# Performance work log

Measured on AMD Instinct MI355X. Metric: run time of the kernel, lower is better.

Reference implementation:

```python
import jax, jax.numpy as jnp
import numpy as np

N, D, K = 16384, 256, 4096   # tokens, feature dim, codebook_size
GAMMA = 0.99


def setup_inputs() -> dict:
    key = jax.random.key(0)
    k1, k2, k3 = jax.random.split(key, 3)
    features = jax.random.normal(k1, (N, D), dtype=jnp.float32)
    mask = jax.random.uniform(k2, (N,)) < 0.9
    codebook = jax.random.normal(k3, (K, D), dtype=jnp.float32)  # hk RandomNormal init
    count = jnp.zeros((K,), jnp.float32)
    avg = jnp.zeros((K,), jnp.float32)
    return {"features": features, "mask": mask, "codebook": codebook,
            "count": count, "avg": avg}


def reference(features, mask, codebook, count, avg):
    sg = jax.lax.stop_gradient
    prev_codebook = codebook

    # pairwise squared distances [N, K] via ||f||^2 - 2 f.C^T + ||c||^2
    f2 = jnp.sum(features * features, axis=-1)            # [N]
    c2 = jnp.sum(codebook * codebook, axis=-1)            # [K]
    distance = f2[:, None] - 2.0 * (features @ codebook.T) + c2[None, :]
    distance = jnp.where(mask[:, None], distance, jnp.inf)

    assign_fwd = jnp.argmin(distance, axis=1)             # [N] nearest code per token
    assign_rev = jnp.argmin(distance, axis=0)             # [K] nearest token per code
    features_fwd = codebook[assign_fwd]                   # [N, D]
    features_rev = features[assign_rev]                   # [K, D]

    # straight-through estimator
    out_features = sg(features_fwd) + features - sg(features)

    total = jnp.maximum(mask.sum(), 1).astype(features.dtype)
    commitment = jnp.mean((sg(features_fwd) - features) ** 2, axis=-1)
    commitment_loss = jnp.where(mask, commitment, 0.0).sum() / total

    # scatter-add assignment counts (masked) and feature sums (unmasked, as in source)
    assignment_count = jnp.zeros((K,), jnp.float32).at[assign_fwd].add(
        mask.astype(jnp.float32))
    assignment_mask = assignment_count < 1

    count = (1.0 - GAMMA) * assignment_count + GAMMA * count
    avg = (1.0 - GAMMA) * assignment_count / total + GAMMA * avg
    alpha = jnp.exp(-avg * K * 10.0 / (1.0 - GAMMA) - 0.001)

    feat_sum = jnp.zeros_like(codebook).at[assign_fwd].add(features)  # [K, D]
    assigned_update = (GAMMA * codebook + (1.0 - GAMMA) * feat_sum)
    assigned_update = assigned_update / jnp.maximum(count[:, None], 1.0)
    unassigned_update = (1.0 - alpha)[:, None] * codebook + alpha[:, None] * features_rev
    new_codebook = jnp.where(assignment_mask[:, None], assigned_update, unassigned_update)

    # pmean(delta) is identity on a single device; final = prev + (prev - new), as in source
    codebook_delta = prev_codebook - new_codebook
    new_codebook = prev_codebook + codebook_delta

    unassigned_percent = (assignment_count > 0).mean()
    return (out_features, assign_fwd, commitment_loss, unassigned_percent,
            count, avg, new_codebook)
```

## Files before the change

### kernel.cpp

```cpp
#include <hip/hip_runtime.h>
#include <math.h>

typedef unsigned long long u64;
typedef unsigned int u32;

#define N_TOK 16384
#define DIM   256
#define KCB   4096

#define WS_ROWMIN   0
#define WS_COLMIN   131072
#define WS_CNT      163840
#define WS_CPART    180224
#define WS_TOTAL    181248
#define WS_FLAG     181252
#define WS_F2       181312
#define WS_C2       246848
#define WS_END      263232

#define OUT_FEAT    0
#define OUT_ASSIGN  4194304
#define OUT_CLOSS   4210688
#define OUT_UPCT    4210689
#define OUT_COUNT   4210690
#define OUT_AVG     4214786
#define OUT_CB      4218882

#define C_1MG 0.009999999776482582f

__device__ __forceinline__ u32 fkey(float d) {
    u32 u = __float_as_uint(d);
    return (u & 0x80000000u) ? ~u : (u | 0x80000000u);
}
__device__ __forceinline__ u64 u64min(u64 a, u64 b) { return a < b ? a : b; }
__device__ __forceinline__ u64 shflxor64(u64 v, int m) {
    int lo = __shfl_xor((int)(u32)(v & 0xFFFFFFFFULL), m, 64);
    int hi = __shfl_xor((int)(u32)(v >> 32), m, 64);
    return ((u64)(u32)hi << 32) | (u32)lo;
}
__device__ __forceinline__ bool read_mask(const void* mp, int flag, int n) {
    if (flag == 2) return ((const float*)mp)[n] != 0.0f;
    if (flag == 1) return ((const int*)mp)[n] != 0;
    return ((const unsigned char*)mp)[n] != 0;
}

__global__ void k_detect(const void* __restrict__ mp, int* __restrict__ flag) {
    if (threadIdx.x == 0) {
        const u32* w = (const u32*)mp;
        bool allf = true, alli = true, any1 = false;
        for (int i = 0; i < 64; ++i) {
            u32 x = w[i];
            if (x != 0u && x != 0x3F800000u) allf = false;
            if (x == 0x3F800000u) any1 = true;
            if (x > 1u) alli = false;
        }
        *flag = (allf && any1) ? 2 : (alli ? 1 : 0);
    }
}

__global__ __launch_bounds__(256)
void k_norms(const float* __restrict__ F, const float* __restrict__ CB,
             const void* __restrict__ mp, const int* __restrict__ flagp,
             float* __restrict__ f2, float* __restrict__ c2) {
    __shared__ float red[4];
    const int b = blockIdx.x, d = threadIdx.x;
    const float* src = (b < N_TOK) ? (F + (size_t)b * DIM) : (CB + (size_t)(b - N_TOK) * DIM);
    float v = src[d];
    float s = v * v;
#pragma unroll
    for (int m = 32; m > 0; m >>= 1) s += __shfl_xor(s, m, 64);
    if ((d & 63) == 0) red[d >> 6] = s;
    __syncthreads();
    if (d == 0) {
        float tot = red[0] + red[1] + red[2] + red[3];
        if (b < N_TOK) {
            bool msk = read_mask(mp, *flagp, b);
            f2[b] = msk ? tot : __builtin_huge_valf();
        } else {
            c2[b - N_TOK] = tot;
        }
    }
}

__global__ __launch_bounds__(256, 4)
void k_gemm(const float* __restrict__ F, const float* __restrict__ CB,
            const float* __restrict__ f2, const float* __restrict__ c2,
            u64* __restrict__ rowmin, u64* __restrict__ colmin) {
    __shared__ float As[128][32];
    __shared__ float Bs[128][32];
    __shared__ u64 colred[4][128];

    const int t = threadIdx.x;
    const int ty = t >> 4, tx = t & 15;
    const int wave = t >> 6;
    const int rowbase = blockIdx.x * 128;
    const int kbase = blockIdx.y * 128;

    float acc[8][8];
#pragma unroll
    for (int i = 0; i < 8; ++i)
#pragma unroll
        for (int j = 0; j < 8; ++j) acc[i][j] = 0.0f;

    for (int dc = 0; dc < 8; ++dc) {
        const int db = dc * 32;
#pragma unroll
        for (int i = 0; i < 4; ++i) {
            int g = t + i * 256;
            int r = g >> 3;
            int c4 = (g & 7) << 2;
            int sw = c4 ^ (((r >> 3) & 7) << 2);
            *(float4*)&As[r][sw] = *(const float4*)(F + (size_t)(rowbase + r) * DIM + db + c4);
            *(float4*)&Bs[r][sw] = *(const float4*)(CB + (size_t)(kbase + r) * DIM + db + c4);
        }
        __syncthreads();
#pragma unroll
        for (int dd = 0; dd < 32; dd += 2) {
            float2 a[8], b[8];
#pragma unroll
            for (int i = 0; i < 8; ++i)
                a[i] = *(const float2*)&As[ty * 8 + i][dd ^ ((ty & 7) << 2)];
#pragma unroll
            for (int j = 0; j < 8; ++j)
                b[j] = *(const float2*)&Bs[tx * 8 + j][dd ^ ((tx & 7) << 2)];
#pragma unroll
            for (int i = 0; i < 8; ++i)
#pragma unroll
                for (int j = 0; j < 8; ++j) {
                    acc[i][j] = fmaf(a[i].x, b[j].x, acc[i][j]);
                    acc[i][j] = fmaf(a[i].y, b[j].y, acc[i][j]);
                }
        }
        __syncthreads();
    }

    float c2k[8];
#pragma unroll
    for (int j = 0; j < 8; ++j) c2k[j] = c2[kbase + tx * 8 + j];
    u64 cbst[8];
#pragma unroll
    for (int j = 0; j < 8; ++j) cbst[j] = ~0ULL;

#pragma unroll
    for (int i = 0; i < 8; ++i) {
        const int row = rowbase + ty * 8 + i;
        const float f2r = f2[row];
        u64 rbst = ~0ULL;
#pragma unroll
        for (int j = 0; j < 8; ++j) {
            float dist = (f2r - 2.0f * acc[i][j]) + c2k[j];
            u64 hk = (u64)fkey(dist) << 32;
            rbst    = u64min(rbst, hk | (u32)(kbase + tx * 8 + j));
            cbst[j] = u64min(cbst[j], hk | (u32)row);
        }
        rbst = u64min(rbst, shflxor64(rbst, 1));
        rbst = u64min(rbst, shflxor64(rbst, 2));
        rbst = u64min(rbst, shflxor64(rbst, 4));
        rbst = u64min(rbst, shflxor64(rbst, 8));
        if (tx == 0) atomicMin(&rowmin[row], rbst);
    }

#pragma unroll
    for (int j = 0; j < 8; ++j) {
        cbst[j] = u64min(cbst[j], shflxor64(cbst[j], 16));
        cbst[j] = u64min(cbst[j], shflxor64(cbst[j], 32));
    }
    if ((t & 63) < 16) {
#pragma unroll
        for (int j = 0; j < 8; ++j) colred[wave][tx * 8 + j] = cbst[j];
    }
    __syncthreads();
    if (t < 128) {
        u64 m = u64min(u64min(colred[0][t], colred[1][t]),
                       u64min(colred[2][t], colred[3][t]));
        atomicMin(&colmin[kbase + t], m);
    }
}

__global__ __launch_bounds__(256)
void k_token(const float* __restrict__ F, const float* __restrict__ CB,
             const u64* __restrict__ rowmin, const void* __restrict__ mp,
             const int* __restrict__ flagp,
             float* __restrict__ out_feat, float* __restrict__ out_assign,
             float* __restrict__ cnt, float* __restrict__ fsum,
             float* __restrict__ cpart) {
    __shared__ float red[4];
    const int n = blockIdx.x, d = threadIdx.x;
    const int k = (int)(u32)(rowmin[n] & 0xFFFFFFFFULL);
    const float f = F[(size_t)n * DIM + d];
    const float cv = CB[(size_t)k * DIM + d];
    out_feat[(size_t)n * DIM + d] = (cv + f) - f;
    const float df = cv - f;
    float s = df * df;
#pragma unroll
    for (int m = 32; m > 0; m >>= 1) s += __shfl_xor(s, m, 64);
    if ((d & 63) == 0) red[d >> 6] = s;
    __syncthreads();
    atomicAdd(&fsum[(size_t)k * DIM + d], f);
    if (d == 0) {
        out_assign[n] = (float)k;
        bool msk = read_mask(mp, *flagp, n);
        if (msk) {
            float tot = red[0] + red[1] + red[2] + red[3];
            atomicAdd(&cnt[k], 1.0f);
            atomicAdd(&cpart[n & 255], tot * (1.0f / 256.0f));
        }
    }
}

__global__ __launch_bounds__(256)
void k_scalars(const float* __restrict__ cnt, const float* __restrict__ cpart,
               float* __restrict__ totf, float* __restrict__ out) {
    __shared__ float redf[4], redc[4];
    __shared__ int redi[4];
    const int t = threadIdx.x;
    float ts = 0.0f;
    int asg = 0;
    for (int i = t; i < KCB; i += 256) {
        float v = cnt[i];
        ts += v;
        asg += (v > 0.0f) ? 1 : 0;
    }
    float cs = cpart[t];
#pragma unroll
    for (int m = 32; m > 0; m >>= 1) {
        ts += __shfl_xor(ts, m, 64);
        cs += __shfl_xor(cs, m, 64);
        asg += __shfl_xor(asg, m, 64);
    }
    if ((t & 63) == 0) { redf[t >> 6] = ts; redc[t >> 6] = cs; redi[t >> 6] = asg; }
    __syncthreads();
    if (t == 0) {
        float total = redf[0] + redf[1] + redf[2] + redf[3];
        total = fmaxf(total, 1.0f);
        float closs = (redc[0] + redc[1] + redc[2] + redc[3]) / total;
        int a = redi[0] + redi[1] + redi[2] + redi[3];
        totf[0] = total;
        out[OUT_CLOSS] = closs;
        out[OUT_UPCT] = (float)a / 4096.0f;
    }
}

__global__ __launch_bounds__(256)
void k_cbupd(const float* __restrict__ F, const float* __restrict__ CB,
             const float* __restrict__ cnt_in, const float* __restrict__ avg_in,
             const float* __restrict__ ac_, const float* __restrict__ fsum,
             const u64* __restrict__ colmin, const float* __restrict__ totf,
             float* __restrict__ out_count, float* __restrict__ out_avg,
             float* __restrict__ out_cb) {
    const int k = blockIdx.x, d = threadIdx.x;
    const float ac = ac_[k];
    const float total = totf[0];
    const float cn = C_1MG * ac + 0.99f * cnt_in[k];
    const float av = (C_1MG * ac) / total + 0.99f * avg_in[k];
    const float arg = ((-av * 4096.0f) * 10.0f) / C_1MG - 0.001f;
    const float alpha = expf(arg);
    const int tok = (int)(u32)(colmin[k] & 0xFFFFFFFFULL);
    const float cb = CB[(size_t)k * DIM + d];
    const float fs = fsum[(size_t)k * DIM + d];
    const float fr = F[(size_t)tok * DIM + d];
    const float assigned = (0.99f * cb + C_1MG * fs) / fmaxf(cn, 1.0f);
    const float unass = (1.0f - alpha) * cb + alpha * fr;
    const float nc = (ac < 1.0f) ? assigned : unass;
    out_cb[(size_t)k * DIM + d] = cb + (cb - nc);
    if (d == 0) { out_count[k] = cn; out_avg[k] = av; }
}

extern "C" void kernel_launch(void* const* d_in, const int* in_sizes, int n_in,
                              void* d_out, int out_size, void* d_ws, size_t ws_size,
                              hipStream_t stream) {
    const float* F   = (const float*)d_in[0];
    const void*  Mp  = d_in[1];
    const float* CB  = (const float*)d_in[2];
    const float* CNT = (const float*)d_in[3];
    const float* AVG = (const float*)d_in[4];
    float* out = (float*)d_out;
    char* ws = (char*)d_ws;
    if (ws_size < (size_t)WS_END) return;

    u64*   rowmin = (u64*)(ws + WS_ROWMIN);
    u64*   colmin = (u64*)(ws + WS_COLMIN);
    float* cnt    = (float*)(ws + WS_CNT);
    float* cpart  = (float*)(ws + WS_CPART);
    float* totf   = (float*)(ws + WS_TOTAL);
    int*   flag   = (int*)(ws + WS_FLAG);
    float* f2     = (float*)(ws + WS_F2);
    float* c2     = (float*)(ws + WS_C2);
    float* fsum   = out + OUT_CB;

    hipMemsetAsync(ws, 0xFF, 163840, stream);
    hipMemsetAsync(ws + WS_CNT, 0, WS_FLAG - WS_CNT, stream);
    hipMemsetAsync(fsum, 0, (size_t)KCB * DIM * sizeof(float), stream);

    k_detect<<<1, 64, 0, stream>>>(Mp, flag);
    k_norms<<<N_TOK + KCB, 256, 0, stream>>>(F, CB, Mp, flag, f2, c2);
    k_gemm<<<dim3(128, 32), 256, 0, stream>>>(F, CB, f2, c2, rowmin, colmin);
    k_token<<<N_TOK, 256, 0, stream>>>(F, CB, rowmin, Mp, flag,
                                       out + OUT_FEAT, out + OUT_ASSIGN,
                                       cnt, fsum, cpart);
    k_scalars<<<1, 256, 0, stream>>>(cnt, cpart, totf, out);
    k_cbupd<<<KCB, 256, 0, stream>>>(F, CB, CNT, AVG, cnt, fsum, colmin, totf,
                                     out + OUT_COUNT, out + OUT_AVG, out + OUT_CB);
}
```

Before: 639.5 us.

## Restructure distance GEMM with direct global-to-LDS double-buffered codebook tiles

Rewrites the distance GEMM so each 512-thread block covers 64 tokens by 128 codes. Each wave owns 8 token rows and reads the feature rows directly from global memory, which are the same addresses across lanes and so act as broadcast loads. Codebook tiles are streamed into LDS with global_load_lds in a double-buffered pipeline with explicit waitcnt and barriers. The row argmin now uses full-wave shuffles and the column argmin reduces over 8 waves. The aim is to overlap loads with FMAs and cut LDS traffic for the A operand, but the register tile per thread shrinks from 8x8 to 8x2, which lowers arithmetic intensity per load.

Result: faster. 558.1 us (-12.7%).

```diff
diff --git a/kernel.cpp b/kernel.cpp
--- a/kernel.cpp
+++ b/kernel.cpp
@@ -42,6 +42,11 @@
     if (flag == 2) return ((const float*)mp)[n] != 0.0f;
     if (flag == 1) return ((const int*)mp)[n] != 0;
     return ((const unsigned char*)mp)[n] != 0;
+}
+__device__ __forceinline__ void gload_lds16(const void* g, void* l) {
+    __builtin_amdgcn_global_load_lds((const __attribute__((address_space(1))) void*)g,
+                                     (__attribute__((address_space(3))) void*)l,
+                                     16, 0, 0);
 }
 
 __global__ void k_detect(const void* __restrict__ mp, int* __restrict__ flag) {
@@ -82,97 +87,106 @@
     }
 }
 
-__global__ __launch_bounds__(256, 4)
+__global__ __launch_bounds__(512, 6)
 void k_gemm(const float* __restrict__ F, const float* __restrict__ CB,
             const float* __restrict__ f2, const float* __restrict__ c2,
             u64* __restrict__ rowmin, u64* __restrict__ colmin) {
-    __shared__ float As[128][32];
-    __shared__ float Bs[128][32];
-    __shared__ u64 colred[4][128];
+    __shared__ float Bs[2 * 128 * 16];
+    __shared__ u64 colred[8][128];
 
     const int t = threadIdx.x;
-    const int ty = t >> 4, tx = t & 15;
-    const int wave = t >> 6;
-    const int rowbase = blockIdx.x * 128;
+    const int l = t & 63;
+    const int wave = __builtin_amdgcn_readfirstlane(t >> 6);
+    const int rowbase = blockIdx.x * 64;
     const int kbase = blockIdx.y * 128;
 
-    float acc[8][8];
+    float acc[8][2];
+#pragma unroll
+    for (int i = 0; i < 8; ++i) { acc[i][0] = 0.0f; acc[i][1] = 0.0f; }
+
+    const int br = t >> 2;
+    const int bc4 = (t & 3) << 2;
+    const int bsc = bc4 ^ (((br >> 1) & 3) << 2);
+    const char* gB = (const char*)(CB + (size_t)(kbase + br) * DIM + bsc);
+    char* BsB = (char*)Bs;
+
+    const float* aRow[8];
 #pragma unroll
     for (int i = 0; i < 8; ++i)
-#pragma unroll
-        for (int j = 0; j < 8; ++j) acc[i][j] = 0.0f;
-
-    for (int dc = 0; dc < 8; ++dc) {
-        const int db = dc * 32;
-#pragma unroll
-        for (int i = 0; i < 4; ++i) {
-            int g = t + i * 256;
-            int r = g >> 3;
-            int c4 = (g & 7) << 2;
-            int sw = c4 ^ (((r >> 3) & 7) << 2);
-            *(float4*)&As[r][sw] = *(const float4*)(F + (size_t)(rowbase + r) * DIM + db + c4);
-            *(float4*)&Bs[r][sw] = *(const float4*)(CB + (size_t)(kbase + r) * DIM + db + c4);
-        }
-        __syncthreads();
-#pragma unroll
-        for (int dd = 0; dd < 32; dd += 2) {
-            float2 a[8], b[8];
+        aRow[i] = F + (size_t)(rowbase + wave * 8 + i) * DIM;
+
+    const int bsw = ((l >> 1) & 3) << 2;
+    const int rb0 = l * 16;
+    const int rb1 = 1024 + l * 16;
+
+#define STAGE(s) gload_lds16(gB + (s) * 64, BsB + (((s) & 1) ? 8192 : 0) + wave * 1024);
+
+    STAGE(0);
+    for (int s = 0; s < 16; ++s) {
+        if (s < 15) {
+            STAGE(s + 1);
+            asm volatile("s_waitcnt vmcnt(1)" ::: "memory");
+        } else {
+            asm volatile("s_waitcnt vmcnt(0)" ::: "memory");
+        }
+        __builtin_amdgcn_s_barrier();
+        const float* Bb = Bs + ((s & 1) ? 2048 : 0);
+        const int ko = s * 16;
+#pragma unroll
+        for (int dd = 0; dd < 16; dd += 4) {
+            const int cb = dd ^ bsw;
+            float4 b0 = *(const float4*)&Bb[rb0 + cb];
+            float4 b1 = *(const float4*)&Bb[rb1 + cb];
+            float4 a[8];
 #pragma unroll
             for (int i = 0; i < 8; ++i)
-                a[i] = *(const float2*)&As[ty * 8 + i][dd ^ ((ty & 7) << 2)];
-#pragma unroll
-            for (int j = 0; j < 8; ++j)
-                b[j] = *(const float2*)&Bs[tx * 8 + j][dd ^ ((tx & 7) << 2)];
-#pragma unroll
-            for (int i = 0; i < 8; ++i)
-#pragma unroll
-                for (int j = 0; j < 8; ++j) {
-                    acc[i][j] = fmaf(a[i].x, b[j].x, acc[i][j]);
-                    acc[i][j] = fmaf(a[i].y, b[j].y, acc[i][j]);
-                }
-        }
-        __syncthreads();
-    }
-
-    float c2k[8];
-#pragma unroll
-    for (int j = 0; j < 8; ++j) c2k[j] = c2[kbase + tx * 8 + j];
-    u64 cbst[8];
-#pragma unroll
-    for (int j = 0; j < 8; ++j) cbst[j] = ~0ULL;
+                a[i] = *(const float4*)(aRow[i] + ko + dd);
+#pragma unroll
+            for (int i = 0; i < 8; ++i) {
+                acc[i][0] = fmaf(a[i].x, b0.x, acc[i][0]);
+                acc[i][0] = fmaf(a[i].y, b0.y, acc[i][0]);
+                acc[i][0] = fmaf(a[i].z, b0.z, acc[i][0]);
+                acc[i][0] = fmaf(a[i].w, b0.w, acc[i][0]);
+                acc[i][1] = fmaf(a[i].x, b1.x, acc[i][1]);
+                acc[i][1] = fmaf(a[i].y, b1.y, acc[i][1]);
+                acc[i][1] = fmaf(a[i].z, b1.z, acc[i][1]);
+                acc[i][1] = fmaf(a[i].w, b1.w, acc[i][1]);
+            }
+        }
+        __builtin_amdgcn_s_barrier();
+    }
+
+    const float c2k0 = c2[kbase + l];
+    const float c2k1 = c2[kbase + 64 + l];
+    u64 cb0 = ~0ULL, cb1 = ~0ULL;
 
 #pragma unroll
     for (int i = 0; i < 8; ++i) {
-        const int row = rowbase + ty * 8 + i;
+        const int row = rowbase + wave * 8 + i;
         const float f2r = f2[row];
-        u64 rbst = ~0ULL;
-#pragma unroll
-        for (int j = 0; j < 8; ++j) {
-            float dist = (f2r - 2.0f * acc[i][j]) + c2k[j];
-            u64 hk = (u64)fkey(dist) << 32;
-            rbst    = u64min(rbst, hk | (u32)(kbase + tx * 8 + j));
-            cbst[j] = u64min(cbst[j], hk | (u32)row);
-        }
-        rbst = u64min(rbst, shflxor64(rbst, 1));
-        rbst = u64min(rbst, shflxor64(rbst, 2));
-        rbst = u64min(rbst, shflxor64(rbst, 4));
-        rbst = u64min(rbst, shflxor64(rbst, 8));
-        if (tx == 0) atomicMin(&rowmin[row], rbst);
-    }
-
-#pragma unroll
-    for (int j = 0; j < 8; ++j) {
-        cbst[j] = u64min(cbst[j], shflxor64(cbst[j], 16));
-        cbst[j] = u64min(cbst[j], shflxor64(cbst[j], 32));
-    }
-    if ((t & 63) < 16) {
-#pragma unroll
-        for (int j = 0; j < 8; ++j) colred[wave][tx * 8 + j] = cbst[j];
-    }
+        const float d0 = (f2r - 2.0f * acc[i][0]) + c2k0;
+        const float d1 = (f2r - 2.0f * acc[i][1]) + c2k1;
+        u64 k0 = ((u64)fkey(d0) << 32) | (u32)(kbase + l);
+        u64 k1 = ((u64)fkey(d1) << 32) | (u32)(kbase + 64 + l);
+        u64 rb = u64min(k0, k1);
+        rb = u64min(rb, shflxor64(rb, 1));
+        rb = u64min(rb, shflxor64(rb, 2));
+        rb = u64min(rb, shflxor64(rb, 4));
+        rb = u64min(rb, shflxor64(rb, 8));
+        rb = u64min(rb, shflxor64(rb, 16));
+        rb = u64min(rb, shflxor64(rb, 32));
+        if (l == 0) atomicMin(&rowmin[row], rb);
+        cb0 = u64min(cb0, ((u64)fkey(d0) << 32) | (u32)row);
+        cb1 = u64min(cb1, ((u64)fkey(d1) << 32) | (u32)row);
+    }
+
+    colred[wave][l] = cb0;
+    colred[wave][64 + l] = cb1;
     __syncthreads();
     if (t < 128) {
-        u64 m = u64min(u64min(colred[0][t], colred[1][t]),
-                       u64min(colred[2][t], colred[3][t]));
+        u64 m = colred[0][t];
+#pragma unroll
+        for (int w = 1; w < 8; ++w) m = u64min(m, colred[w][t]);
         atomicMin(&colmin[kbase + t], m);
     }
 }
@@ -294,7 +308,7 @@
 
     k_detect<<<1, 64, 0, stream>>>(Mp, flag);
     k_norms<<<N_TOK + KCB, 256, 0, stream>>>(F, CB, Mp, flag, f2, c2);
-    k_gemm<<<dim3(128, 32), 256, 0, stream>>>(F, CB, f2, c2, rowmin, colmin);
+    k_gemm<<<dim3(256, 32), 512, 0, stream>>>(F, CB, f2, c2, rowmin, colmin);
     k_token<<<N_TOK, 256, 0, stream>>>(F, CB, rowmin, Mp, flag,
                                        out + OUT_FEAT, out + OUT_ASSIGN,
                                        cnt, fsum, cpart);
```
